# Performance work log

Measured on AMD Instinct MI355X. Metric: run time of the kernel, lower is better.

Reference implementation:

```python
import jax, jax.numpy as jnp
import numpy as np

B, N, N2 = 4, 4096, 4096
CIN, DIM, KNN, UP = 128, 64, 20, 2
HPOS, HATT = 64, 256
EPS = 1e-5


def _group(feat, idx):
    # feat: (B,C,M), idx: (B,N,K) -> (B,C,N,K) gather of neighbor features
    return jax.vmap(lambda f, i: f[:, i])(feat, idx)


def _conv1d(w, b, x):
    # 1x1 Conv1d: w (O,C), x (B,C,N)
    return jnp.einsum('oc,bcn->bon', w, x) + b[:, None]


def _bn(x, g, be, m, v):
    # eval-mode BatchNorm2d on (B,C,N,K)
    inv = g / jnp.sqrt(v + EPS)
    return x * inv[:, None, None] + (be - m * inv)[:, None, None]


def setup_inputs() -> dict:
    key = jax.random.key(0)
    ks = jax.random.split(key, 32)
    r = lambda i, s: jax.random.normal(ks[i], s, jnp.float32)
    u = lambda i, s: jax.random.uniform(ks[i], s, jnp.float32, 0.5, 1.5)
    return {
        'pos1': r(0, (B, 3, N)),
        'query': r(1, (B, CIN, N)),
        'pos2': r(2, (B, 3, N2)),
        'key_feat': r(3, (B, CIN, N2)),
        'wq': r(4, (DIM, CIN)) * 0.05, 'bq': r(5, (DIM,)) * 0.05,
        'wk': r(6, (DIM, CIN)) * 0.05, 'bk': r(7, (DIM,)) * 0.05,
        'wv': r(8, (DIM, CIN)) * 0.05, 'bv': r(9, (DIM,)) * 0.05,
        'pw1': r(10, (HPOS, 3)) * 0.2, 'pb1': r(11, (HPOS,)) * 0.05,
        'pg': u(12, (HPOS,)), 'pbt': r(13, (HPOS,)) * 0.05,
        'pm': r(14, (HPOS,)) * 0.05, 'pv': u(15, (HPOS,)),
        'pw2': r(16, (DIM, HPOS)) * 0.1, 'pb2': r(17, (DIM,)) * 0.05,
        'aw1': r(18, (HATT, DIM)) * 0.1, 'ab1': r(19, (HATT,)) * 0.05,
        'ag': u(20, (HATT,)), 'abt2': r(21, (HATT,)) * 0.05,
        'am': r(22, (HATT,)) * 0.05, 'av': u(23, (HATT,)),
        'awt': r(24, (HATT, DIM, UP)) * 0.05, 'abt': r(25, (DIM,)) * 0.05,
        'we': r(26, (CIN, DIM)) * 0.1, 'be': r(27, (CIN,)) * 0.05,
    }


def reference(pos1, query, pos2, key_feat, wq, bq, wk, bk, wv, bv,
              pw1, pb1, pg, pbt, pm, pv, pw2, pb2,
              aw1, ab1, ag, abt2, am, av, awt, abt, we, be):
    q = _conv1d(wq, bq, query)          # (B,DIM,N)
    k = _conv1d(wk, bk, key_feat)       # (B,DIM,N2)
    v = _conv1d(wv, bv, key_feat)       # (B,DIM,N2)
    # KNN of pos1 queries into pos2 support set
    p1 = pos1.transpose(0, 2, 1)        # (B,N,3)
    p2 = pos2.transpose(0, 2, 1)        # (B,N2,3)
    d = (jnp.sum(p1 * p1, -1)[:, :, None] + jnp.sum(p2 * p2, -1)[:, None, :]
         - 2.0 * jnp.einsum('bnd,bmd->bnm', p1, p2))
    _, idx = jax.lax.top_k(-d, KNN)     # (B,N,KNN)
    kg = _group(k, idx)                 # (B,DIM,N,K)
    qk_rel = q[:, :, :, None] - kg
    pos_rel = pos1[:, :, :, None] - _group(pos2, idx)   # (B,3,N,K)
    # pos_mlp: conv2d 3->HPOS, BN, ReLU, conv2d HPOS->DIM
    pe = jnp.einsum('oc,bcnk->bonk', pw1, pos_rel) + pb1[:, None, None]
    pe = jax.nn.relu(_bn(pe, pg, pbt, pm, pv))
    pe = jnp.einsum('oc,bcnk->bonk', pw2, pe) + pb2[:, None, None]  # (B,DIM,N,K)
    # attn_mlp: conv2d DIM->HATT, BN, ReLU, ConvTranspose2d HATT->DIM kernel (UP,1)
    h = qk_rel + pe
    a = jnp.einsum('oc,bcnk->bonk', aw1, h) + ab1[:, None, None]
    a = jax.nn.relu(_bn(a, ag, abt2, am, av))               # (B,HATT,N,K)
    att = jnp.einsum('bcnk,cor->bonrk', a, awt).reshape(B, DIM, N * UP, KNN)
    att = att + abt[:, None, None]
    att = jax.nn.softmax(att, axis=-1)
    vg = _group(v, idx) + pe            # (B,DIM,N,K)
    vu = jnp.repeat(vg, UP, axis=2)     # nearest upsample -> (B,DIM,N*UP,K)
    agg = jnp.sum(att * vu, axis=-1)    # (B,DIM,N*UP)
    y = _conv1d(we, be, agg)            # (B,CIN,N*UP)
    identity = jnp.repeat(query, UP, axis=2)  # residual (in==out -> Identity)
    return y + identity
```

## Files before the change

kernel.cpp:

```cpp
#include <hip/hip_runtime.h>
#include <hip/hip_bf16.h>

#define BATCH 4
#define NPTS  4096
#define NPTS2 4096
#define CIN   128
#define DIM   64
#define KNN   20
#define UPF   2
#define HPOS  64
#define HATT  256
#define MOUT  8192
#define EPSF  1e-5f
#define QPB   6
#define BPB   683

#define FB_KNN   1024
#define FB_PKV   (FB_KNN + 256)
#define FB_PQ    (FB_PKV + 256)
#define FB_PACK  (FB_PQ + 128)

typedef _Float16 h16x8 __attribute__((ext_vector_type(8)));
typedef _Float16 h16x4 __attribute__((ext_vector_type(4)));
typedef _Float16 h16x2 __attribute__((ext_vector_type(2)));
typedef float    f32x4 __attribute__((ext_vector_type(4)));

__device__ inline float rdlane(float v, int src) {
  return __int_as_float(__builtin_amdgcn_readlane(__float_as_int(v), src));
}

__device__ __forceinline__ float distf(float qn, float m2x, float m2y, float m2z,
                                       float x, float y, float z) {
  float s = __fmaf_rn(x, x, qn);
  s = __fmaf_rn(y, y, s);
  s = __fmaf_rn(z, z, s);
  s = __fmaf_rn(m2x, x, s);
  s = __fmaf_rn(m2y, y, s);
  s = __fmaf_rn(m2z, z, s);
  return s;
}

__global__ __launch_bounds__(256) void front(
    const float* __restrict__ pos1, const float* __restrict__ pos2,
    int* __restrict__ idxout,
    const float* __restrict__ key_feat,
    const float* __restrict__ wk, const float* __restrict__ bk,
    const float* __restrict__ wv, const float* __restrict__ bv,
    float* __restrict__ k_t, float* __restrict__ v_t,
    const float* __restrict__ query,
    const float* __restrict__ wq, const float* __restrict__ bq,
    float* __restrict__ q_t,
    const float* __restrict__ aw1, const float* __restrict__ awt,
    const float* __restrict__ pw2,
    const float* __restrict__ ag,  const float* __restrict__ av,
    const float* __restrict__ abt2, const float* __restrict__ am,
    const float* __restrict__ abt,
    const float* __restrict__ pg,  const float* __restrict__ pv,
    const float* __restrict__ pbt, const float* __restrict__ pm,
    const float* __restrict__ ab1, const float* __restrict__ pb1,
    const float* __restrict__ pw1,
    _Float16* __restrict__ aw1h, _Float16* __restrict__ awtP,
    _Float16* __restrict__ pw2h, float* __restrict__ abtX,
    float* __restrict__ ab1f, float* __restrict__ pw1f,
    float* __restrict__ pb1f) {
  __shared__ union {
    struct { float X[CIN][64]; float O[64][65]; } pj;
    struct { int cnt[16]; float dbuf[16][64]; int jbuf[16][64]; } kn;
  } smU;
  const int bid = blockIdx.x;
  const int t   = threadIdx.x;

  if (bid < FB_KNN) {
    const int lane = t & 63;
    const int wv   = t >> 6;
    const int b    = bid >> 8;
    const int nb   = (bid & 255) * 16;
    const float* p2x = pos2 + (b * 3 + 0) * NPTS2;
    const float* p2y = pos2 + (b * 3 + 1) * NPTS2;
    const float* p2z = pos2 + (b * 3 + 2) * NPTS2;

    float qn[4], m2x[4], m2y[4], m2z[4];
#pragma unroll
    for (int qi = 0; qi < 4; ++qi) {
      int n = nb + wv * 4 + qi;
      float qx = pos1[(b * 3 + 0) * NPTS + n];
      float qy = pos1[(b * 3 + 1) * NPTS + n];
      float qz = pos1[(b * 3 + 2) * NPTS + n];
      qn[qi]  = qx * qx + qy * qy + qz * qz;
      m2x[qi] = -2.0f * qx; m2y[qi] = -2.0f * qy; m2z[qi] = -2.0f * qz;
    }

    float mymin[4] = {3.402823466e38f, 3.402823466e38f,
                      3.402823466e38f, 3.402823466e38f};
    f32x4 cx[4], cy[4], cz[4];
#pragma unroll 1
    for (int c = 0; c < 4; ++c) {
      int base = c * 1024 + lane * 4;
#pragma unroll
      for (int g = 0; g < 4; ++g) {
        cx[g] = *(const f32x4*)(p2x + base + g * 256);
        cy[g] = *(const f32x4*)(p2y + base + g * 256);
        cz[g] = *(const f32x4*)(p2z + base + g * 256);
      }
#pragma unroll
      for (int qi = 0; qi < 4; ++qi)
#pragma unroll
        for (int g = 0; g < 4; ++g)
#pragma unroll
          for (int e = 0; e < 4; ++e) {
            float d = distf(qn[qi], m2x[qi], m2y[qi], m2z[qi],
                            cx[g][e], cy[g][e], cz[g][e]);
            mymin[qi] = fminf(mymin[qi], d);
          }
    }

    float T0[4];
#pragma unroll
    for (int qi = 0; qi < 4; ++qi) {
      float v = mymin[qi];
#pragma unroll
      for (int k = 2; k <= 64; k <<= 1)
#pragma unroll
        for (int jj = k >> 1; jj >= 1; jj >>= 1) {
          float o = __shfl_xor(v, jj);
          bool up = ((lane & k) == 0);
          bool keepmin = (((lane & jj) == 0) == up);
          v = keepmin ? fminf(v, o) : fmaxf(v, o);
        }
      T0[qi] = rdlane(v, 19);
    }

    if (lane < 4) smU.kn.cnt[wv * 4 + lane] = 0;

#pragma unroll 1
    for (int c = 0; c < 4; ++c) {
      int base = c * 1024 + lane * 4;
#pragma unroll
      for (int g = 0; g < 4; ++g) {
        cx[g] = *(const f32x4*)(p2x + base + g * 256);
        cy[g] = *(const f32x4*)(p2y + base + g * 256);
        cz[g] = *(const f32x4*)(p2z + base + g * 256);
      }
#pragma unroll
      for (int qi = 0; qi < 4; ++qi) {
        const int qq = wv * 4 + qi;
#pragma unroll
        for (int g = 0; g < 4; ++g)
#pragma unroll
          for (int e = 0; e < 4; ++e) {
            float d = distf(qn[qi], m2x[qi], m2y[qi], m2z[qi],
                            cx[g][e], cy[g][e], cz[g][e]);
            if (d <= T0[qi]) {
              int slot = atomicAdd(&smU.kn.cnt[qq], 1);
              if (slot < 64) { smU.kn.dbuf[qq][slot] = d; smU.kn.jbuf[qq][slot] = base + g * 256 + e; }
            }
          }
      }
    }

#pragma unroll 1
    for (int qi = 0; qi < 4; ++qi) {
      const int qq = wv * 4 + qi;
      const int n  = nb + qq;
      const int cnt = smU.kn.cnt[qq];
      if (cnt <= 64) {
        float dk = (lane < cnt) ? smU.kn.dbuf[qq][lane] : 3.402823466e38f;
        int   jk = (lane < cnt) ? smU.kn.jbuf[qq][lane] : 0x7fffffff;
#pragma unroll
        for (int k = 2; k <= 64; k <<= 1) {
#pragma unroll
          for (int jj = k >> 1; jj >= 1; jj >>= 1) {
            float od = __shfl_xor(dk, jj);
            int   oj = __shfl_xor(jk, jj);
            bool mineSm = (dk < od) || (dk == od && jk < oj);
            bool up = ((lane & k) == 0);
            bool keepmin = (((lane & jj) == 0) == up);
            bool takeOther = (keepmin != mineSm);
            dk = takeOther ? od : dk;
            jk = takeOther ? oj : jk;
          }
        }
        if (lane < KNN) idxout[(b * NPTS + n) * KNN + lane] = jk;
      } else {
        float dl = 3.402823466e38f;
        int   il = 0;
        for (int j0 = 0; j0 < NPTS2; j0 += 64) {
          int j = j0 + lane;
          float d = distf(qn[qi], m2x[qi], m2y[qi], m2z[qi], p2x[j], p2y[j], p2z[j]);
          float T = rdlane(dl, 19);
          unsigned long long m = __ballot(d < T);
          while (m) {
            int src = __ffsll(m) - 1;
            m &= m - 1;
            float dd = rdlane(d, src);
            float T2 = rdlane(dl, 19);
            if (dd < T2) {
              int jj2 = j0 + src;
              float pd = __shfl_up(dl, 1);
              int   pi = __shfl_up(il, 1);
              if (dl > dd) {
                if (lane == 0 || pd <= dd) { dl = dd; il = jj2; }
                else                       { dl = pd; il = pi; }
              }
            }
          }
        }
        if (lane < KNN) idxout[(b * NPTS + n) * KNN + lane] = il;
      }
    }
  } else if (bid < FB_PKV) {
    const int vb = bid - FB_KNN;
    const int b  = vb >> 6;
    const int n0 = (vb & 63) * 64;
    for (int l = t; l < CIN * 64; l += 256) {
      int c = l >> 6, i = l & 63;
      smU.pj.X[c][i] = key_feat[(b * CIN + c) * NPTS2 + n0 + i];
    }
    __syncthreads();
    const int n_l = t & 63;
    const int w   = __builtin_amdgcn_readfirstlane(t >> 6);
    float acck[16], accv[16];
#pragma unroll
    for (int i = 0; i < 16; ++i) { acck[i] = bk[w * 16 + i]; accv[i] = bv[w * 16 + i]; }
    for (int c = 0; c < CIN; ++c) {
      float xv = smU.pj.X[c][n_l];
#pragma unroll
      for (int i = 0; i < 16; ++i) {
        acck[i] += wk[(w * 16 + i) * CIN + c] * xv;
        accv[i] += wv[(w * 16 + i) * CIN + c] * xv;
      }
    }
#pragma unroll
    for (int i = 0; i < 16; ++i) smU.pj.O[n_l][w * 16 + i] = acck[i];
    __syncthreads();
    for (int l = t; l < 64 * 64; l += 256)
      k_t[(b * NPTS2 + n0 + (l >> 6)) * DIM + (l & 63)] = smU.pj.O[l >> 6][l & 63];
    __syncthreads();
#pragma unroll
    for (int i = 0; i < 16; ++i) smU.pj.O[n_l][w * 16 + i] = accv[i];
    __syncthreads();
    for (int l = t; l < 64 * 64; l += 256)
      v_t[(b * NPTS2 + n0 + (l >> 6)) * DIM + (l & 63)] = smU.pj.O[l >> 6][l & 63];
  } else if (bid < FB_PQ) {
    const int vb = bid - FB_PKV;
    const int b  = vb >> 6;
    const int n0 = (vb & 63) * 64;
    for (int l = t; l < CIN * 64; l += 256) {
      int c = l >> 6, i = l & 63;
      smU.pj.X[c][i] = query[(b * CIN + c) * NPTS + n0 + i];
    }
    __syncthreads();
    const int n_l = t & 63;
    const int w   = __builtin_amdgcn_readfirstlane(t >> 6);
    float acc[16];
#pragma unroll
    for (int i = 0; i < 16; ++i) acc[i] = bq[w * 16 + i];
    for (int c = 0; c < CIN; ++c) {
      float xv = smU.pj.X[c][n_l];
#pragma unroll
      for (int i = 0; i < 16; ++i) acc[i] += wq[(w * 16 + i) * CIN + c] * xv;
    }
#pragma unroll
    for (int i = 0; i < 16; ++i) smU.pj.O[n_l][w * 16 + i] = acc[i];
    __syncthreads();
    for (int l = t; l < 64 * 64; l += 256)
      q_t[(b * NPTS + n0 + (l >> 6)) * DIM + (l & 63)] = smU.pj.O[l >> 6][l & 63];
  } else {
    int i = (bid - FB_PQ) * 256 + t;
    if (i < 16384) {
      int j = i >> 6;
      float inv = ag[j] / sqrtf(av[j] + EPSF);
      aw1h[i] = (_Float16)(aw1[i] * inv);
    }
    if (i < 32768) {
      int orr = i >> 8, j = i & 255;
      awtP[i] = (_Float16)awt[j * 128 + orr];
    }
    if (i < 4096) pw2h[i] = (_Float16)pw2[i];
    if (i < 256) {
      float inv = ag[i] / sqrtf(av[i] + EPSF);
      ab1f[i] = ab1[i] * inv + (abt2[i] - am[i] * inv);
    }
    if (i < 192) {
      int hc = i / 3;
      float inv = pg[hc] / sqrtf(pv[hc] + EPSF);
      pw1f[i] = pw1[i] * inv;
    }
    if (i < 128) abtX[i] = abt[i >> 1];
    if (i < 64) {
      float inv = pg[i] / sqrtf(pv[i] + EPSF);
      pb1f[i] = pb1[i] * inv + (pbt[i] - pm[i] * inv);
    }
  }
}

#define SM_R0    0
#define SM_R1    18432
#define SM_LGC   0
#define SM_VGB   36864

__global__ __launch_bounds__(256, 3) void attn_mfma(
    const float* __restrict__ q_t, const float* __restrict__ k_t,
    const float* __restrict__ v_t, const int* __restrict__ idx,
    const float* __restrict__ pos1, const float* __restrict__ pos2,
    const float* __restrict__ pw1f, const float* __restrict__ pb1f,
    const _Float16* __restrict__ pw2h, const float* __restrict__ pb2,
    const _Float16* __restrict__ aw1h, const float* __restrict__ ab1f,
    const _Float16* __restrict__ awtP, const float* __restrict__ abtX,
    float* __restrict__ agg) {
  __shared__ __align__(16) char smem[54272];
  const int b  = blockIdx.x / BPB;
  const int n0 = (blockIdx.x - b * BPB) * QPB;
  const int t  = threadIdx.x;
  const int lane = t & 63;
  const int w  = t >> 6;
  const int r  = lane & 15;
  const int q4 = lane >> 4;
  const int c0 = t & 63;
  const int cgB = w;

  int  jBh[2]; bool okh[2]; int nqh[2];
#pragma unroll
  for (int hl = 0; hl < 2; ++hl) {
    int colB = c0 + hl * 64;
    int pB = colB / 20;
    okh[hl] = (pB < QPB) && (n0 + pB < NPTS);
    nqh[hl] = okh[hl] ? (n0 + pB) : 0;
    jBh[hl] = okh[hl] ? idx[(b * NPTS + nqh[hl]) * KNN + (colB - pB * 20)] : 0;
  }

  f32x4 qk4[4], vv4[4];
  {
    const float* qrow = q_t + ((size_t)(b * NPTS  + nqh[0])) * DIM + cgB * 16;
    const float* krow = k_t + ((size_t)(b * NPTS2 + jBh[0])) * DIM + cgB * 16;
    const float* vrow = v_t + ((size_t)(b * NPTS2 + jBh[0])) * DIM + cgB * 16;
#pragma unroll
    for (int u = 0; u < 4; ++u) {
      f32x4 qv = *(const f32x4*)(qrow + u * 4);
      f32x4 kv = *(const f32x4*)(krow + u * 4);
      qk4[u] = qv - kv;
      vv4[u] = *(const f32x4*)(vrow + u * 4);
    }
  }

#pragma unroll
  for (int hl = 0; hl < 2; ++hl) {
    int colB = c0 + hl * 64;
    float p0 = 0.f, p1 = 0.f, p2 = 0.f;
    if (okh[hl]) {
      p0 = pos1[(b * 3 + 0) * NPTS + nqh[hl]] - pos2[(b * 3 + 0) * NPTS2 + jBh[hl]];
      p1 = pos1[(b * 3 + 1) * NPTS + nqh[hl]] - pos2[(b * 3 + 1) * NPTS2 + jBh[hl]];
      p2 = pos1[(b * 3 + 2) * NPTS + nqh[hl]] - pos2[(b * 3 + 2) * NPTS2 + jBh[hl]];
    }
#pragma unroll
    for (int hf = 0; hf < 2; ++hf) {
      h16x8 pk;
#pragma unroll
      for (int ii = 0; ii < 8; ++ii) {
        int hc = cgB * 16 + hf * 8 + ii;
        float v0 = pb1f[hc] + pw1f[hc*3] * p0 + pw1f[hc*3+1] * p1 + pw1f[hc*3+2] * p2;
        v0 = fmaxf(v0, 0.f);
        if (!okh[hl]) v0 = 0.f;
        pk[ii] = (_Float16)v0;
      }
      *(h16x8*)(smem + SM_R0 + ((colB * 72 + cgB * 16 + hf * 8) * 2)) = pk;
    }
  }
  __syncthreads();

  {
    f32x4 acc[8];
#pragma unroll
    for (int nt = 0; nt < 8; ++nt) acc[nt] = (f32x4){0.f, 0.f, 0.f, 0.f};
#pragma unroll
    for (int ks = 0; ks < 2; ++ks) {
      h16x8 a0 = *(const h16x8*)&pw2h[(w * 16 + r) * 64 + ks * 32 + q4 * 8];
#pragma unroll
      for (int nt = 0; nt < 8; ++nt) {
        h16x8 bv = *(h16x8*)(smem + SM_R0 + ((nt * 16 + r) * 72 + ks * 32 + q4 * 8) * 2);
        acc[nt] = __builtin_amdgcn_mfma_f32_16x16x32_f16(a0, bv, acc[nt], 0, 0, 0);
      }
    }
    int o0 = w * 16 + q4 * 4;
    f32x4 pbv = *(const f32x4*)&pb2[o0];
#pragma unroll
    for (int nt = 0; nt < 8; ++nt) {
      f32x4 vv = acc[nt] + pbv;
      h16x4 pk = {(_Float16)vv[0], (_Float16)vv[1], (_Float16)vv[2], (_Float16)vv[3]};
      *(h16x4*)(smem + SM_R1 + ((nt * 16 + r) * 72 + o0) * 2) = pk;
    }
  }

#pragma unroll 1
  for (int hl = 0; hl < 2; ++hl) {
    int colB = c0 + hl * 64;
    if (hl == 1) {
      const float* qrow = q_t + ((size_t)(b * NPTS  + nqh[1])) * DIM + cgB * 16;
      const float* krow = k_t + ((size_t)(b * NPTS2 + jBh[1])) * DIM + cgB * 16;
      const float* vrow = v_t + ((size_t)(b * NPTS2 + jBh[1])) * DIM + cgB * 16;
#pragma unroll
      for (int u = 0; u < 4; ++u) {
        f32x4 qv = *(const f32x4*)(qrow + u * 4);
        f32x4 kv = *(const f32x4*)(krow + u * 4);
        qk4[u] = qv - kv;
        vv4[u] = *(const f32x4*)(vrow + u * 4);
      }
    }
    h16x8 pe8[2];
#pragma unroll
    for (int hf = 0; hf < 2; ++hf)
      pe8[hf] = *(h16x8*)(smem + SM_R1 + (colB * 72 + cgB * 16 + hf * 8) * 2);
    h16x8 hp8[2];
#pragma unroll
    for (int u = 0; u < 4; ++u) {
      int hf = u >> 1, e0 = (u & 1) * 4;
      f32x4 pe = {(float)pe8[hf][e0],     (float)pe8[hf][e0 + 1],
                  (float)pe8[hf][e0 + 2], (float)pe8[hf][e0 + 3]};
      f32x4 hv = qk4[u] + pe;
      f32x4 gv = vv4[u] + pe;
      if (!okh[hl]) { hv = (f32x4){0.f,0.f,0.f,0.f}; gv = hv; }
      hp8[hf][e0]     = (_Float16)hv[0];
      hp8[hf][e0 + 1] = (_Float16)hv[1];
      hp8[hf][e0 + 2] = (_Float16)hv[2];
      hp8[hf][e0 + 3] = (_Float16)hv[3];
      h16x4 gp = {(_Float16)gv[0], (_Float16)gv[1], (_Float16)gv[2], (_Float16)gv[3]};
      *(h16x4*)(smem + SM_VGB + (colB * 68 + cgB * 16 + u * 4) * 2) = gp;
    }
#pragma unroll
    for (int hf = 0; hf < 2; ++hf)
      *(h16x8*)(smem + SM_R1 + (colB * 72 + cgB * 16 + hf * 8) * 2) = hp8[hf];
  }
  __syncthreads();

  f32x4 accD[2][8];
#pragma unroll
  for (int h = 0; h < 2; ++h)
#pragma unroll
    for (int nt = 0; nt < 8; ++nt) accD[h][nt] = (f32x4){0.f, 0.f, 0.f, 0.f};

#define C_QUARTER(quar)                                                        \
  {                                                                            \
    int mt = (quar) * 4 + w;                                                   \
    f32x4 acc[8];                                                              \
    _Pragma("unroll")                                                          \
    for (int nt = 0; nt < 8; ++nt) acc[nt] = (f32x4){0.f, 0.f, 0.f, 0.f};      \
    _Pragma("unroll")                                                          \
    for (int ks = 0; ks < 2; ++ks) {                                           \
      h16x8 af = *(const h16x8*)&aw1h[(mt * 16 + r) * 64 + ks * 32 + q4 * 8];  \
      h16x8 bsv[8];                                                            \
      _Pragma("unroll")                                                        \
      for (int nt = 0; nt < 8; ++nt)                                           \
        bsv[nt] = *(h16x8*)(smem + SM_R1 + ((nt * 16 + r) * 72 + ks * 32 + q4 * 8) * 2); \
      _Pragma("unroll")                                                        \
      for (int nt = 0; nt < 8; ++nt)                                           \
        acc[nt] = __builtin_amdgcn_mfma_f32_16x16x32_f16(af, bsv[nt], acc[nt], 0, 0, 0); \
    }                                                                          \
    int j0  = mt * 16 + q4 * 4;                                                \
    int jq0 = j0 - (quar) * 64;                                                \
    f32x4 b1 = *(const f32x4*)&ab1f[j0];                                       \
    _Pragma("unroll")                                                          \
    for (int nt = 0; nt < 8; ++nt) {                                           \
      int col = nt * 16 + r;                                                   \
      float v0 = fmaxf(acc[nt][0] + b1[0], 0.f);                               \
      float v1 = fmaxf(acc[nt][1] + b1[1], 0.f);                               \
      float v2 = fmaxf(acc[nt][2] + b1[2], 0.f);                               \
      float v3 = fmaxf(acc[nt][3] + b1[3], 0.f);                               \
      h16x4 pk = {(_Float16)v0, (_Float16)v1, (_Float16)v2, (_Float16)v3};     \
      *(h16x4*)(smem + SM_R0 + (col * 72 + jq0) * 2) = pk;                     \
    }                                                                          \
  }

#define D_QUARTER(quar)                                                        \
  {                                                                            \
    _Pragma("unroll")                                                          \
    for (int ks2 = 0; ks2 < 2; ++ks2) {                                        \
      h16x8 bsv[8];                                                            \
      _Pragma("unroll")                                                        \
      for (int nt = 0; nt < 8; ++nt)                                           \
        bsv[nt] = *(h16x8*)(smem + SM_R0 + ((nt * 16 + r) * 72 + ks2 * 32 + q4 * 8) * 2); \
      int ksg = (quar) * 2 + ks2;                                              \
      _Pragma("unroll")                                                        \
      for (int h = 0; h < 2; ++h) {                                            \
        int mt2 = w * 2 + h;                                                   \
        h16x8 af = *(const h16x8*)&awtP[(mt2 * 16 + r) * 256 + ksg * 32 + q4 * 8]; \
        _Pragma("unroll")                                                      \
        for (int nt = 0; nt < 8; ++nt)                                         \
          accD[h][nt] = __builtin_amdgcn_mfma_f32_16x16x32_f16(af, bsv[nt], accD[h][nt], 0, 0, 0); \
      }                                                                        \
    }                                                                          \
  }

  C_QUARTER(0)
  __syncthreads();
  D_QUARTER(0)
  __syncthreads();
  C_QUARTER(1)
  __syncthreads();
  D_QUARTER(1)
  __syncthreads();
  C_QUARTER(2)
  __syncthreads();
  D_QUARTER(2)
  __syncthreads();
  C_QUARTER(3)
  __syncthreads();
  D_QUARTER(3)
  __syncthreads();

  {
#pragma unroll
    for (int h = 0; h < 2; ++h) {
      int orr0 = (w * 2 + h) * 16 + q4 * 4;
      f32x4 ab = *(const f32x4*)&abtX[orr0];
#pragma unroll
      for (int nt = 0; nt < 8; ++nt) {
        int col = nt * 16 + r;
        if (col < QPB * KNN) {
          f32x4 vv = accD[h][nt] + ab;
          h16x4 pk = {(_Float16)vv[0], (_Float16)vv[1], (_Float16)vv[2], (_Float16)vv[3]};
          *(h16x4*)(smem + SM_LGC + (col * 136 + orr0) * 2) = pk;
        }
      }
    }
  }
  __syncthreads();

#pragma unroll 1
  for (int it = 0; it < 2; ++it) {
    int p  = (t >> 6) + it * 4;
    int li = t & 63;
    if (p < QPB && n0 + p < NPTS) {
      h16x2 Lp[KNN];
      float G[KNN];
#pragma unroll
      for (int kk = 0; kk < KNN; ++kk) {
        Lp[kk] = *(h16x2*)(smem + SM_LGC + ((p * 20 + kk) * 136 + li * 2) * 2);
        G[kk]  = (float)*(_Float16*)(smem + SM_VGB + ((p * 20 + kk) * 68 + li) * 2);
      }
#pragma unroll
      for (int half = 0; half < 2; ++half) {
        float mx = (float)Lp[0][half];
#pragma unroll
        for (int kk = 1; kk < KNN; ++kk) mx = fmaxf(mx, (float)Lp[kk][half]);
        float s = 0.f, a = 0.f;
#pragma unroll
        for (int kk = 0; kk < KNN; ++kk) {
          float e = __expf((float)Lp[kk][half] - mx);
          s += e;
          a += e * G[kk];
        }
        float rs = 1.0f / s;
        agg[(((size_t)(b * NPTS + n0 + p)) * UPF + half) * DIM + li] = a * rs;
      }
    }
  }
#undef C_QUARTER
#undef D_QUARTER
}

__global__ __launch_bounds__(256) void out_proj(const float* __restrict__ agg,
    const float* __restrict__ we, const float* __restrict__ be,
    const float* __restrict__ query, float* __restrict__ out) {
  __shared__ float A[64][65];
  const int b  = blockIdx.x >> 7;
  const int m0 = (blockIdx.x & 127) * 64;
  const int t  = threadIdx.x;
  for (int l = t; l < 64 * 64; l += 256) {
    int row = l >> 6, c = l & 63;
    A[row][c] = agg[(b * MOUT + m0 + row) * DIM + c];
  }
  __syncthreads();
  const int m_l = t & 63;
  const int w   = __builtin_amdgcn_readfirstlane(t >> 6);
  float acc[32];
#pragma unroll
  for (int i = 0; i < 32; ++i) acc[i] = 0.f;
  for (int c = 0; c < DIM; ++c) {
    float a = A[m_l][c];
#pragma unroll
    for (int i = 0; i < 32; ++i) acc[i] += we[(w * 32 + i) * DIM + c] * a;
  }
  const int m = m0 + m_l;
#pragma unroll
  for (int i = 0; i < 32; ++i) {
    int o = w * 32 + i;
    out[(b * CIN + o) * MOUT + m] = acc[i] + be[o] + query[(b * CIN + o) * NPTS + (m >> 1)];
  }
}

extern "C" void kernel_launch(void* const* d_in, const int* in_sizes, int n_in,
                              void* d_out, int out_size, void* d_ws, size_t ws_size,
                              hipStream_t stream) {
  (void)in_sizes; (void)n_in; (void)out_size; (void)ws_size;
  const float* pos1     = (const float*)d_in[0];
  const float* query    = (const float*)d_in[1];
  const float* pos2     = (const float*)d_in[2];
  const float* key_feat = (const float*)d_in[3];
  const float* wq  = (const float*)d_in[4];
  const float* bq  = (const float*)d_in[5];
  const float* wk  = (const float*)d_in[6];
  const float* bk  = (const float*)d_in[7];
  const float* wv  = (const float*)d_in[8];
  const float* bv  = (const float*)d_in[9];
  const float* pw1 = (const float*)d_in[10];
  const float* pb1 = (const float*)d_in[11];
  const float* pg  = (const float*)d_in[12];
  const float* pbt = (const float*)d_in[13];
  const float* pm  = (const float*)d_in[14];
  const float* pv  = (const float*)d_in[15];
  const float* pw2 = (const float*)d_in[16];
  const float* pb2 = (const float*)d_in[17];
  const float* aw1 = (const float*)d_in[18];
  const float* ab1 = (const float*)d_in[19];
  const float* ag  = (const float*)d_in[20];
  const float* abt2= (const float*)d_in[21];
  const float* am  = (const float*)d_in[22];
  const float* av  = (const float*)d_in[23];
  const float* awt = (const float*)d_in[24];
  const float* abt = (const float*)d_in[25];
  const float* we  = (const float*)d_in[26];
  const float* be  = (const float*)d_in[27];

  float* ws   = (float*)d_ws;
  float* q_t  = ws;
  float* k_t  = q_t + BATCH * NPTS * DIM;
  float* v_t  = k_t + BATCH * NPTS2 * DIM;
  float* aggb = v_t + BATCH * NPTS2 * DIM;
  int*   idxb = (int*)(aggb + BATCH * MOUT * DIM);
  _Float16* aw1h = (_Float16*)(idxb + BATCH * NPTS * KNN);
  _Float16* awtP = aw1h + HATT * DIM;
  _Float16* pw2h = awtP + 128 * HATT;
  float* abtX    = (float*)(pw2h + DIM * HPOS);
  float* ab1f    = abtX + 128;
  float* pw1f    = ab1f + HATT;
  float* pb1f    = pw1f + HPOS * 3;

  front<<<FB_PACK, 256, 0, stream>>>(
      pos1, pos2, idxb,
      key_feat, wk, bk, wv, bv, k_t, v_t,
      query, wq, bq, q_t,
      aw1, awt, pw2, ag, av, abt2, am, abt,
      pg, pv, pbt, pm, ab1, pb1, pw1,
      aw1h, awtP, pw2h, abtX, ab1f, pw1f, pb1f);
  attn_mfma<<<BATCH * BPB, 256, 0, stream>>>(q_t, k_t, v_t, idxb, pos1, pos2,
      pw1f, pb1f, pw2h, pb2, aw1h, ab1f, awtP, abtX, aggb);
  out_proj<<<BATCH * (MOUT / 64), 256, 0, stream>>>(aggb, we, be, query, (float*)d_out);
}
```

Measured before the change: 314.4 us.

## Double-buffer attention hidden activations in LDS to halve block barriers

The attention MLP's intermediate activations now alternate between two LDS buffers across quarters. The next quarter's first GEMM can therefore write while the previous quarter's second GEMM still reads, which removes every other __syncthreads in the C/D pipeline. The cost is more shared memory (about 54 KB up to about 72 KB per block), and launch bounds drop from 3 to 2 blocks per CU, so occupancy falls. Less latency can then be hidden across blocks.

After: 310.0 us (median of 2 runs). No clear change (-1.4%).

```diff
diff --git a/kernel.cpp b/kernel.cpp
--- a/kernel.cpp
+++ b/kernel.cpp
@@ -294,12 +294,14 @@
   }
 }
 
-#define SM_R0    0
-#define SM_R1    18432
+#define SM_HB    0
+#define SM_H1B   18432
+#define SM_AL0   18432
+#define SM_AL1   36864
+#define SM_VGB   55296
 #define SM_LGC   0
-#define SM_VGB   36864
-
-__global__ __launch_bounds__(256, 3) void attn_mfma(
+
+__global__ __launch_bounds__(256, 2) void attn_mfma(
     const float* __restrict__ q_t, const float* __restrict__ k_t,
     const float* __restrict__ v_t, const int* __restrict__ idx,
     const float* __restrict__ pos1, const float* __restrict__ pos2,
@@ -308,7 +310,7 @@
     const _Float16* __restrict__ aw1h, const float* __restrict__ ab1f,
     const _Float16* __restrict__ awtP, const float* __restrict__ abtX,
     float* __restrict__ agg) {
-  __shared__ __align__(16) char smem[54272];
+  __shared__ __align__(16) char smem[72704];
   const int b  = blockIdx.x / BPB;
   const int n0 = (blockIdx.x - b * BPB) * QPB;
   const int t  = threadIdx.x;
@@ -363,7 +365,7 @@
         if (!okh[hl]) v0 = 0.f;
         pk[ii] = (_Float16)v0;
       }
-      *(h16x8*)(smem + SM_R0 + ((colB * 72 + cgB * 16 + hf * 8) * 2)) = pk;
+      *(h16x8*)(smem + SM_H1B + ((colB * 72 + cgB * 16 + hf * 8) * 2)) = pk;
     }
   }
   __syncthreads();
@@ -377,7 +379,7 @@
       h16x8 a0 = *(const h16x8*)&pw2h[(w * 16 + r) * 64 + ks * 32 + q4 * 8];
 #pragma unroll
       for (int nt = 0; nt < 8; ++nt) {
-        h16x8 bv = *(h16x8*)(smem + SM_R0 + ((nt * 16 + r) * 72 + ks * 32 + q4 * 8) * 2);
+        h16x8 bv = *(h16x8*)(smem + SM_H1B + ((nt * 16 + r) * 72 + ks * 32 + q4 * 8) * 2);
         acc[nt] = __builtin_amdgcn_mfma_f32_16x16x32_f16(a0, bv, acc[nt], 0, 0, 0);
       }
     }
@@ -387,7 +389,7 @@
     for (int nt = 0; nt < 8; ++nt) {
       f32x4 vv = acc[nt] + pbv;
       h16x4 pk = {(_Float16)vv[0], (_Float16)vv[1], (_Float16)vv[2], (_Float16)vv[3]};
-      *(h16x4*)(smem + SM_R1 + ((nt * 16 + r) * 72 + o0) * 2) = pk;
+      *(h16x4*)(smem + SM_HB + ((nt * 16 + r) * 72 + o0) * 2) = pk;
     }
   }
 
@@ -409,7 +411,7 @@
     h16x8 pe8[2];
 #pragma unroll
     for (int hf = 0; hf < 2; ++hf)
-      pe8[hf] = *(h16x8*)(smem + SM_R1 + (colB * 72 + cgB * 16 + hf * 8) * 2);
+      pe8[hf] = *(h16x8*)(smem + SM_HB + (colB * 72 + cgB * 16 + hf * 8) * 2);
     h16x8 hp8[2];
 #pragma unroll
     for (int u = 0; u < 4; ++u) {
@@ -428,7 +430,7 @@
     }
 #pragma unroll
     for (int hf = 0; hf < 2; ++hf)
-      *(h16x8*)(smem + SM_R1 + (colB * 72 + cgB * 16 + hf * 8) * 2) = hp8[hf];
+      *(h16x8*)(smem + SM_HB + (colB * 72 + cgB * 16 + hf * 8) * 2) = hp8[hf];
   }
   __syncthreads();
 
@@ -438,7 +440,7 @@
 #pragma unroll
     for (int nt = 0; nt < 8; ++nt) accD[h][nt] = (f32x4){0.f, 0.f, 0.f, 0.f};
 
-#define C_QUARTER(quar)                                                        \
+#define C_QUARTER(quar, albase)                                                \
   {                                                                            \
     int mt = (quar) * 4 + w;                                                   \
     f32x4 acc[8];                                                              \
@@ -450,7 +452,7 @@
       h16x8 bsv[8];                                                            \
       _Pragma("unroll")                                                        \
       for (int nt = 0; nt < 8; ++nt)                                           \
-        bsv[nt] = *(h16x8*)(smem + SM_R1 + ((nt * 16 + r) * 72 + ks * 32 + q4 * 8) * 2); \
+        bsv[nt] = *(h16x8*)(smem + SM_HB + ((nt * 16 + r) * 72 + ks * 32 + q4 * 8) * 2); \
       _Pragma("unroll")                                                        \
       for (int nt = 0; nt < 8; ++nt)                                           \
         acc[nt] = __builtin_amdgcn_mfma_f32_16x16x32_f16(af, bsv[nt], acc[nt], 0, 0, 0); \
@@ -466,18 +468,18 @@
       float v2 = fmaxf(acc[nt][2] + b1[2], 0.f);                               \
       float v3 = fmaxf(acc[nt][3] + b1[3], 0.f);                               \
       h16x4 pk = {(_Float16)v0, (_Float16)v1, (_Float16)v2, (_Float16)v3};     \
-      *(h16x4*)(smem + SM_R0 + (col * 72 + jq0) * 2) = pk;                     \
+      *(h16x4*)(smem + (albase) + (col * 72 + jq0) * 2) = pk;                  \
     }                                                                          \
   }
 
-#define D_QUARTER(quar)                                                        \
+#define D_QUARTER(quar, albase)                                                \
   {                                                                            \
     _Pragma("unroll")                                                          \
     for (int ks2 = 0; ks2 < 2; ++ks2) {                                        \
       h16x8 bsv[8];                                                            \
       _Pragma("unroll")                                                        \
       for (int nt = 0; nt < 8; ++nt)                                           \
-        bsv[nt] = *(h16x8*)(smem + SM_R0 + ((nt * 16 + r) * 72 + ks2 * 32 + q4 * 8) * 2); \
+        bsv[nt] = *(h16x8*)(smem + (albase) + ((nt * 16 + r) * 72 + ks2 * 32 + q4 * 8) * 2); \
       int ksg = (quar) * 2 + ks2;                                              \
       _Pragma("unroll")                                                        \
       for (int h = 0; h < 2; ++h) {                                            \
@@ -490,22 +492,18 @@
     }                                                                          \
   }
 
-  C_QUARTER(0)
-  __syncthreads();
-  D_QUARTER(0)
-  __syncthreads();
-  C_QUARTER(1)
-  __syncthreads();
-  D_QUARTER(1)
-  __syncthreads();
-  C_QUARTER(2)
-  __syncthreads();
-  D_QUARTER(2)
-  __syncthreads();
-  C_QUARTER(3)
-  __syncthreads();
-  D_QUARTER(3)
-  __syncthreads();
+  C_QUARTER(0, SM_AL0)
+  __syncthreads();
+  D_QUARTER(0, SM_AL0)
+  C_QUARTER(1, SM_AL1)
+  __syncthreads();
+  D_QUARTER(1, SM_AL1)
+  C_QUARTER(2, SM_AL0)
+  __syncthreads();
+  D_QUARTER(2, SM_AL0)
+  C_QUARTER(3, SM_AL1)
+  __syncthreads();
+  D_QUARTER(3, SM_AL1)
 
   {
 #pragma unroll
```
